# Kernel tuning notes

Hardware: AMD Instinct MI355X
Metric: run time of the kernel (lower is better)

Reference implementation:

```python
import jax, jax.numpy as jnp
import numpy as np

N_NODES = 10000
N_EDGES = 320000
CH = 64          # multiplicity per irrep (64x0e node feats)
R_DIM = 8        # radial embedding dim
L_MAX = 2
N_L = L_MAX + 1
SH_DIM = 9       # 1 + 3 + 5
AVG_NEIGH = 32.0
MLP_HID = 64


def setup_inputs() -> dict:
    key = jax.random.key(0)
    ks = jax.random.split(key, 11)
    return {
        "edge_vectors": jax.random.normal(ks[0], (N_EDGES, 3), jnp.float32),
        "node_feats": jax.random.normal(ks[1], (N_NODES, CH), jnp.float32),
        "radial_embeddings": jax.random.normal(ks[2], (N_EDGES, R_DIM), jnp.float32),
        "senders": jax.random.randint(ks[3], (N_EDGES,), 0, N_NODES),
        "receivers": jax.random.randint(ks[4], (N_EDGES,), 0, N_NODES),
        # learned params (e3nn Linear / MLP weights, unit normal init)
        "W_up": jax.random.normal(ks[5], (CH, CH), jnp.float32),
        "W_mlp1": jax.random.normal(ks[6], (R_DIM, MLP_HID), jnp.float32),
        "W_mlp2": jax.random.normal(ks[7], (MLP_HID, MLP_HID), jnp.float32),
        "W_mlp3": jax.random.normal(ks[8], (MLP_HID, MLP_HID), jnp.float32),
        "W_mlp4": jax.random.normal(ks[9], (MLP_HID, N_L * CH), jnp.float32),
        "W_down": jax.random.normal(ks[10], (N_L, CH, CH), jnp.float32),
    }


def spherical_harmonics(vec):
    """Component-normalized real spherical harmonics (||Y_l||^2 = 2l+1), l=0..2,
    on normalized edge vectors (e3nn normalize=True, normalization='component')."""
    v = vec / jnp.linalg.norm(vec, axis=-1, keepdims=True)
    x, y, z = v[..., 0], v[..., 1], v[..., 2]
    c15 = float(np.sqrt(15.0))
    c5 = float(np.sqrt(5.0))
    sh2 = jnp.stack(
        [c15 * x * y, c15 * y * z, 0.5 * c5 * (3.0 * z * z - 1.0),
         c15 * x * z, 0.5 * c15 * (x * x - y * y)], axis=-1)
    return jnp.concatenate(
        [jnp.ones_like(x)[..., None], float(np.sqrt(3.0)) * v, sh2], axis=-1)  # [E, 9]


def reference(edge_vectors, node_feats, radial_embeddings, senders, receivers,
              W_up, W_mlp1, W_mlp2, W_mlp3, W_mlp4, W_down):
    inv_ch = 1.0 / np.sqrt(CH)
    n_nodes = node_feats.shape[0]

    # linear_up: scalar irreps -> plain channel mixing with e3nn 1/sqrt(fan_in)
    h = (node_feats @ W_up) * inv_ch                               # [N, CH]

    sh = spherical_harmonics(edge_vectors)                         # [E, 9]

    # radial MLP -> one weight per (channel, l) tensor-product path
    m = radial_embeddings
    for W in (W_mlp1, W_mlp2, W_mlp3):
        m = jax.nn.silu((m @ W) / np.sqrt(W.shape[0]))
    mix = (m @ W_mlp4) / np.sqrt(MLP_HID)                          # [E, N_L*CH]
    w = mix.reshape(-1, N_L, CH).transpose(0, 2, 1)                # [E, CH, N_L]
    # broadcast each per-irrep weight over its 2l+1 components
    w = jnp.repeat(w, np.array([1, 3, 5]), axis=-1,
                   total_repeat_length=SH_DIM)                     # [E, CH, 9]

    # tensor product (scalar node feats x Y_l) with radial weights: messages
    msg = h[senders][:, :, None] * sh[:, None, :] * w              # [E, CH, 9]

    # scatter-add to receivers, normalize by avg_num_neighbors
    agg = jax.ops.segment_sum(msg.reshape(msg.shape[0], -1),
                              receivers, num_segments=n_nodes)
    agg = (agg / AVG_NEIGH).reshape(n_nodes, CH, SH_DIM)           # [N, CH, 9]

    # linear_down: independent channel mixing per l (equivariant Linear)
    outs = []
    start = 0
    for l in range(N_L):
        d = 2 * l + 1
        o = jnp.einsum('ncm,cd->ndm', agg[:, :, start:start + d], W_down[l]) * inv_ch
        outs.append(o.reshape(n_nodes, -1))
        start += d
    return jnp.concatenate(outs, axis=-1)                          # [N, 576]
```

## Files before the change

kernel.cpp:

```cpp
#include <hip/hip_runtime.h>
#include <hip/hip_bf16.h>
#include <math.h>

#define N_NODES 10000
#define N_EDGES 320000
#define CH 64
#define MIXW 192
#define EREC 16

#define W1_OFF 0
#define W2_OFF 512
#define W3_OFF 5120
#define W4_OFF 9728
#define W_TOT 23552
#define ACT_STRIDE 72

#define EPB 128

#define PREP_BLKS 92
#define H_BLKS 2500
#define HIST_BLKS 1250

typedef __attribute__((ext_vector_type(8))) short bf16x8;
typedef __attribute__((ext_vector_type(4))) float f32x4;
#define MFMA16(a, b, c) __builtin_amdgcn_mfma_f32_16x16x32_bf16(a, b, c, 0, 0, 0)

__device__ __forceinline__ float bf2f(unsigned short u) {
    union { unsigned int i; float f; } v; v.i = ((unsigned int)u) << 16; return v.f;
}
__device__ __forceinline__ unsigned short f2bf(float f) {
    unsigned int x = __float_as_uint(f);
    unsigned int r = x + 0x7fffu + ((x >> 16) & 1u);
    return (unsigned short)(r >> 16);
}
__device__ __forceinline__ float silu(float t) {
    return t / (1.0f + __expf(-t));
}

__global__ __launch_bounds__(256) void k_pre(const float* __restrict__ W1,
                                             const float* __restrict__ W2,
                                             const float* __restrict__ W3,
                                             const float* __restrict__ W4,
                                             unsigned short* __restrict__ wimg,
                                             const float* __restrict__ nf,
                                             const float* __restrict__ Wup,
                                             float* __restrict__ h,
                                             const int* __restrict__ recv,
                                             int* __restrict__ counts) {
    int bid = blockIdx.x;
    int t = threadIdx.x;
    if (bid < PREP_BLKS) {
        int i = bid * 256 + t;
        if (i >= W_TOT) return;
        float v;
        if (i < W2_OFF) {
            int n = i >> 3, k = i & 7;
            v = W1[k * 64 + n];
        } else if (i < W3_OFF) {
            int j = i - W2_OFF; int n = j / 72, k = j % 72;
            v = (k < 64) ? W2[k * 64 + n] : 0.f;
        } else if (i < W4_OFF) {
            int j = i - W3_OFF; int n = j / 72, k = j % 72;
            v = (k < 64) ? W3[k * 64 + n] : 0.f;
        } else {
            int j = i - W4_OFF; int n = j / 72, k = j % 72;
            v = (k < 64) ? W4[k * MIXW + n] : 0.f;
        }
        wimg[i] = f2bf(v);
    } else if (bid < PREP_BLKS + H_BLKS) {
        int node = __builtin_amdgcn_readfirstlane((bid - PREP_BLKS) * 4 + (t >> 6));
        int lane = t & 63;
        const float* nrow = nf + (size_t)node * CH;
        float acc = 0.f;
#pragma unroll
        for (int k = 0; k < CH; ++k) acc += nrow[k] * Wup[k * CH + lane];
        h[(size_t)node * CH + lane] = acc * 0.125f;
    } else {
        int e = (bid - PREP_BLKS - H_BLKS) * 256 + t;
        atomicAdd(&counts[recv[e]], 1);
    }
}

__global__ __launch_bounds__(1024) void k_scan(const int* __restrict__ counts,
                                               int* __restrict__ offsets,
                                               int* __restrict__ cursor) {
    __shared__ int part[1024];
    int t = threadIdx.x;
    const int CHUNK = 10;
    int base = t * CHUNK;
    int s = 0;
    for (int i = 0; i < CHUNK; ++i) {
        int idx = base + i;
        if (idx < N_NODES) s += counts[idx];
    }
    part[t] = s;
    __syncthreads();
    for (int off = 1; off < 1024; off <<= 1) {
        int v = 0;
        if (t >= off) v = part[t - off];
        __syncthreads();
        part[t] += v;
        __syncthreads();
    }
    int run = part[t] - s;
    for (int i = 0; i < CHUNK; ++i) {
        int idx = base + i;
        if (idx < N_NODES) {
            offsets[idx] = run;
            cursor[idx] = run;
            run += counts[idx];
        }
    }
    if (t == 1023) offsets[N_NODES] = part[1023];
}

__global__ __launch_bounds__(256) void k_scatter(const int* __restrict__ recv,
                                                 int* __restrict__ cursor,
                                                 int* __restrict__ epos) {
    int e = blockIdx.x * 256 + threadIdx.x;
    epos[e] = atomicAdd(&cursor[recv[e]], 1);
}

__global__ __launch_bounds__(256) void k_mlp(const float* __restrict__ ev,
                                             const float* __restrict__ rad,
                                             const unsigned short* __restrict__ wimg,
                                             const int* __restrict__ senders,
                                             const int* __restrict__ epos,
                                             unsigned short* __restrict__ mix,
                                             float* __restrict__ erec) {
    __shared__ unsigned short act[EPB * ACT_STRIDE];
    __shared__ int s_pos[EPB];

    const int t = threadIdx.x;
    const int e0 = blockIdx.x * EPB;
    const int wv = t >> 6;
    const int lane = t & 63;
    const int lrow = lane & 15;
    const int quad = lane >> 4;
    const int wr0 = wv * 32;
    const int em0 = wr0 + lrow;
    const int em1 = em0 + 16;
    const int cr0 = wr0 + quad * 4;
    const int cr1 = cr0 + 16;

    if (lane < 32) s_pos[wr0 + lane] = epos[e0 + wr0 + lane];

    if (t < EPB) {
        int e = e0 + t;
        int p = epos[e];
        float vx = ev[(size_t)e * 3 + 0], vy = ev[(size_t)e * 3 + 1], vz = ev[(size_t)e * 3 + 2];
        float inv = rsqrtf(vx * vx + vy * vy + vz * vz);
        float x = vx * inv, y = vy * inv, z = vz * inv;
        const float s3 = 1.7320508075688772f;
        const float s15 = 3.872983346207417f;
        const float s5 = 2.2360679774997896f;
        float4* rp = (float4*)(erec + (size_t)p * EREC);
        rp[0] = make_float4(1.0f, s3 * x, s3 * y, s3 * z);
        rp[1] = make_float4(s15 * x * y, s15 * y * z, 0.5f * s5 * (3.0f * z * z - 1.0f), s15 * x * z);
        rp[2] = make_float4(0.5f * s15 * (x * x - y * y),
                            __uint_as_float((unsigned)senders[e]), 0.f, 0.f);
        rp[3] = make_float4(0.f, 0.f, 0.f, 0.f);
    }

    bf16x8 ar0 = {0, 0, 0, 0, 0, 0, 0, 0};
    bf16x8 ar1 = {0, 0, 0, 0, 0, 0, 0, 0};
    if (quad == 0) {
        const float4* rp0 = (const float4*)(rad + (size_t)(e0 + em0) * 8);
        const float4* rp1 = (const float4*)(rad + (size_t)(e0 + em1) * 8);
        float4 u = rp0[0], v = rp0[1];
        ar0[0] = (short)f2bf(u.x); ar0[1] = (short)f2bf(u.y);
        ar0[2] = (short)f2bf(u.z); ar0[3] = (short)f2bf(u.w);
        ar0[4] = (short)f2bf(v.x); ar0[5] = (short)f2bf(v.y);
        ar0[6] = (short)f2bf(v.z); ar0[7] = (short)f2bf(v.w);
        u = rp1[0]; v = rp1[1];
        ar1[0] = (short)f2bf(u.x); ar1[1] = (short)f2bf(u.y);
        ar1[2] = (short)f2bf(u.z); ar1[3] = (short)f2bf(u.w);
        ar1[4] = (short)f2bf(v.x); ar1[5] = (short)f2bf(v.y);
        ar1[6] = (short)f2bf(v.z); ar1[7] = (short)f2bf(v.w);
    }

#pragma unroll
    for (int nt = 0; nt < 4; ++nt) {
        bf16x8 bw = {0, 0, 0, 0, 0, 0, 0, 0};
        if (quad == 0) bw = *(const bf16x8*)(wimg + W1_OFF + (nt * 16 + lrow) * 8);
        f32x4 c0 = {0.f, 0.f, 0.f, 0.f};
        f32x4 c1 = {0.f, 0.f, 0.f, 0.f};
        c0 = MFMA16(ar0, bw, c0);
        c1 = MFMA16(ar1, bw, c1);
#pragma unroll
        for (int r = 0; r < 4; ++r) {
            act[(cr0 + r) * ACT_STRIDE + nt * 16 + lrow] =
                (unsigned short)f2bf(silu(c0[r] * 0.3535533905932738f));
            act[(cr1 + r) * ACT_STRIDE + nt * 16 + lrow] =
                (unsigned short)f2bf(silu(c1[r] * 0.3535533905932738f));
        }
    }

#pragma unroll
    for (int L = 0; L < 2; ++L) {
        const unsigned short* wbase = wimg + (L == 0 ? W2_OFF : W3_OFF);
        bf16x8 a00 = *(const bf16x8*)(act + em0 * ACT_STRIDE + quad * 8);
        bf16x8 a01 = *(const bf16x8*)(act + em0 * ACT_STRIDE + 32 + quad * 8);
        bf16x8 a10 = *(const bf16x8*)(act + em1 * ACT_STRIDE + quad * 8);
        bf16x8 a11 = *(const bf16x8*)(act + em1 * ACT_STRIDE + 32 + quad * 8);
        bf16x8 b[4][2];
#pragma unroll
        for (int nt = 0; nt < 4; ++nt)
#pragma unroll
            for (int kh = 0; kh < 2; ++kh)
                b[nt][kh] = *(const bf16x8*)(wbase + (nt * 16 + lrow) * 72 + kh * 32 + quad * 8);
#pragma unroll
        for (int nt = 0; nt < 4; ++nt) {
            f32x4 c0 = {0.f, 0.f, 0.f, 0.f};
            f32x4 c1 = {0.f, 0.f, 0.f, 0.f};
            c0 = MFMA16(a00, b[nt][0], c0);
            c0 = MFMA16(a01, b[nt][1], c0);
            c1 = MFMA16(a10, b[nt][0], c1);
            c1 = MFMA16(a11, b[nt][1], c1);
#pragma unroll
            for (int r = 0; r < 4; ++r) {
                act[(cr0 + r) * ACT_STRIDE + nt * 16 + lrow] =
                    (unsigned short)f2bf(silu(c0[r] * 0.125f));
                act[(cr1 + r) * ACT_STRIDE + nt * 16 + lrow] =
                    (unsigned short)f2bf(silu(c1[r] * 0.125f));
            }
        }
    }

    {
        bf16x8 a00 = *(const bf16x8*)(act + em0 * ACT_STRIDE + quad * 8);
        bf16x8 a01 = *(const bf16x8*)(act + em0 * ACT_STRIDE + 32 + quad * 8);
        bf16x8 a10 = *(const bf16x8*)(act + em1 * ACT_STRIDE + quad * 8);
        bf16x8 a11 = *(const bf16x8*)(act + em1 * ACT_STRIDE + 32 + quad * 8);
#pragma unroll
        for (int T = 0; T < 3; ++T) {
            bf16x8 b[4][2];
#pragma unroll
            for (int ntl = 0; ntl < 4; ++ntl)
#pragma unroll
                for (int kh = 0; kh < 2; ++kh)
                    b[ntl][kh] = *(const bf16x8*)(wimg + W4_OFF +
                        ((T * 4 + ntl) * 16 + lrow) * 72 + kh * 32 + quad * 8);
#pragma unroll
            for (int ntl = 0; ntl < 4; ++ntl) {
                f32x4 c0 = {0.f, 0.f, 0.f, 0.f};
                f32x4 c1 = {0.f, 0.f, 0.f, 0.f};
                c0 = MFMA16(a00, b[ntl][0], c0);
                c0 = MFMA16(a01, b[ntl][1], c0);
                c1 = MFMA16(a10, b[ntl][0], c1);
                c1 = MFMA16(a11, b[ntl][1], c1);
#pragma unroll
                for (int r = 0; r < 4; ++r) {
                    act[(cr0 + r) * ACT_STRIDE + ntl * 16 + lrow] =
                        (unsigned short)f2bf(c0[r] * 0.125f);
                    act[(cr1 + r) * ACT_STRIDE + ntl * 16 + lrow] =
                        (unsigned short)f2bf(c1[r] * 0.125f);
                }
            }
#pragma unroll
            for (int j = 0; j < 4; ++j) {
                int idx = lane + 64 * j;
                int row = idx >> 3, c8 = idx & 7;
                int p = s_pos[wr0 + row];
                uint4 v = *(const uint4*)(act + (wr0 + row) * ACT_STRIDE + c8 * 8);
                *(uint4*)(mix + (size_t)p * MIXW + T * 64 + c8 * 8) = v;
            }
        }
    }
}

__global__ __launch_bounds__(256, 4) void k_aggdown(const int* __restrict__ offsets,
                                                    const float* __restrict__ erec,
                                                    const float* __restrict__ h,
                                                    const unsigned short* __restrict__ mix,
                                                    const float* __restrict__ Wd,
                                                    float* __restrict__ out) {
    __shared__ float sg[4][576];
    int wv = threadIdx.x >> 6;
    int lane = threadIdx.x & 63;
    int node = __builtin_amdgcn_readfirstlane(blockIdx.x * 4 + wv);
    int s0 = __builtin_amdgcn_readfirstlane(offsets[node]);
    int s1 = __builtin_amdgcn_readfirstlane(offsets[node + 1]);
    float acc[9] = {0.f, 0.f, 0.f, 0.f, 0.f, 0.f, 0.f, 0.f, 0.f};
#pragma unroll 4
    for (int i = s0; i < s1; ++i) {
        const float4* rp = (const float4*)(erec + (size_t)i * EREC);
        float4 r0 = rp[0], r1 = rp[1], r2 = rp[2];
        int s = (int)__float_as_uint(r2.y);
        float hv = h[(size_t)s * CH + lane];
        const unsigned short* mrow = mix + (size_t)i * MIXW;
        float w0 = bf2f(mrow[lane]);
        float w1 = bf2f(mrow[64 + lane]);
        float w2 = bf2f(mrow[128 + lane]);
        float h0 = hv * w0, h1 = hv * w1, h2 = hv * w2;
        acc[0] += h0 * r0.x;
        acc[1] += h1 * r0.y;
        acc[2] += h1 * r0.z;
        acc[3] += h1 * r0.w;
        acc[4] += h2 * r1.x;
        acc[5] += h2 * r1.y;
        acc[6] += h2 * r1.z;
        acc[7] += h2 * r1.w;
        acc[8] += h2 * r2.x;
    }
    float* arow = sg[wv];
#pragma unroll
    for (int m = 0; m < 9; ++m) arow[lane * 9 + m] = acc[m] * (1.0f / 32.0f);

    float* orow = out + (size_t)node * 576;
    {
        float a = 0.f;
#pragma unroll
        for (int c = 0; c < 64; ++c) a += arow[c * 9] * Wd[c * 64 + lane];
        orow[lane] = a * 0.125f;
    }
    {
        float m3[3] = {0.f, 0.f, 0.f};
#pragma unroll
        for (int c = 0; c < 64; ++c) {
            float w = Wd[(64 + c) * 64 + lane];
#pragma unroll
            for (int mm = 0; mm < 3; ++mm) m3[mm] += arow[c * 9 + 1 + mm] * w;
        }
#pragma unroll
        for (int mm = 0; mm < 3; ++mm) orow[64 + lane * 3 + mm] = m3[mm] * 0.125f;
    }
    {
        float m5[5] = {0.f, 0.f, 0.f, 0.f, 0.f};
#pragma unroll
        for (int c = 0; c < 64; ++c) {
            float w = Wd[(128 + c) * 64 + lane];
#pragma unroll
            for (int mm = 0; mm < 5; ++mm) m5[mm] += arow[c * 9 + 4 + mm] * w;
        }
#pragma unroll
        for (int mm = 0; mm < 5; ++mm) orow[256 + lane * 5 + mm] = m5[mm] * 0.125f;
    }
}

static inline size_t align256(size_t x) { return (x + 255) & ~(size_t)255; }

extern "C" void kernel_launch(void* const* d_in, const int* in_sizes, int n_in,
                              void* d_out, int out_size, void* d_ws, size_t ws_size,
                              hipStream_t stream) {
    const float* edge_vectors = (const float*)d_in[0];
    const float* node_feats   = (const float*)d_in[1];
    const float* radial       = (const float*)d_in[2];
    const int*   senders      = (const int*)d_in[3];
    const int*   receivers    = (const int*)d_in[4];
    const float* W_up         = (const float*)d_in[5];
    const float* W_mlp1       = (const float*)d_in[6];
    const float* W_mlp2       = (const float*)d_in[7];
    const float* W_mlp3       = (const float*)d_in[8];
    const float* W_mlp4       = (const float*)d_in[9];
    const float* W_down       = (const float*)d_in[10];
    float* out = (float*)d_out;

    char* base = (char*)d_ws;
    size_t off = 0;
    float* h = (float*)(base + off);              off = align256(off + (size_t)N_NODES * CH * 4);
    unsigned short* mix = (unsigned short*)(base + off); off = align256(off + (size_t)N_EDGES * MIXW * 2);
    float* erec = (float*)(base + off);           off = align256(off + (size_t)N_EDGES * EREC * 4);
    unsigned short* wimg = (unsigned short*)(base + off); off = align256(off + (size_t)W_TOT * 2);
    int* epos = (int*)(base + off);               off = align256(off + (size_t)N_EDGES * 4);
    int* counts = (int*)(base + off);             off = align256(off + (size_t)N_NODES * 4);
    int* offsets = (int*)(base + off);            off = align256(off + (size_t)(N_NODES + 1) * 4);
    int* cursor = (int*)(base + off);             off = align256(off + (size_t)N_NODES * 4);

    hipMemsetAsync(counts, 0, (size_t)N_NODES * 4, stream);

    k_pre<<<PREP_BLKS + H_BLKS + HIST_BLKS, 256, 0, stream>>>(
        W_mlp1, W_mlp2, W_mlp3, W_mlp4, wimg, node_feats, W_up, h, receivers, counts);
    k_scan<<<1, 1024, 0, stream>>>(counts, offsets, cursor);
    k_scatter<<<N_EDGES / 256, 256, 0, stream>>>(receivers, cursor, epos);
    k_mlp<<<N_EDGES / EPB, 256, 0, stream>>>(edge_vectors, radial, wimg, senders, epos,
                                             mix, erec);
    k_aggdown<<<N_NODES / 4, 256, 0, stream>>>(offsets, erec, h, mix, W_down, out);
}
```

Before: 251.6 us.

## Fuse scatter into MLP kernel and premultiply sender features into edge weights

Removes the separate scatter kernel: the MLP kernel now does the atomic cursor increment itself to find each edge's sorted position. It gathers sender node features h into shared memory and multiplies them into the radial-MLP output before the bf16 store. The aggregation kernel no longer performs the random h gather or reads a sender index, and the edge record shrinks from 16 to 12 floats. The trade-off is extra shared memory and gathers in the MLP kernel, plus bf16 rounding of the product h*w instead of w alone.

```diff
diff --git a/kernel.cpp b/kernel.cpp
--- a/kernel.cpp
+++ b/kernel.cpp
@@ -6,7 +6,7 @@
 #define N_EDGES 320000
 #define CH 64
 #define MIXW 192
-#define EREC 16
+#define EREC 12
 
 #define W1_OFF 0
 #define W2_OFF 512
@@ -14,6 +14,7 @@
 #define W4_OFF 9728
 #define W_TOT 23552
 #define ACT_STRIDE 72
+#define HROW_STRIDE 66
 
 #define EPB 128
 
@@ -114,22 +115,19 @@
     if (t == 1023) offsets[N_NODES] = part[1023];
 }
 
-__global__ __launch_bounds__(256) void k_scatter(const int* __restrict__ recv,
-                                                 int* __restrict__ cursor,
-                                                 int* __restrict__ epos) {
-    int e = blockIdx.x * 256 + threadIdx.x;
-    epos[e] = atomicAdd(&cursor[recv[e]], 1);
-}
-
 __global__ __launch_bounds__(256) void k_mlp(const float* __restrict__ ev,
                                              const float* __restrict__ rad,
                                              const unsigned short* __restrict__ wimg,
                                              const int* __restrict__ senders,
-                                             const int* __restrict__ epos,
-                                             unsigned short* __restrict__ mix,
+                                             const int* __restrict__ recv,
+                                             int* __restrict__ cursor,
+                                             const float* __restrict__ h,
+                                             unsigned short* __restrict__ hw,
                                              float* __restrict__ erec) {
     __shared__ unsigned short act[EPB * ACT_STRIDE];
+    __shared__ float s_hrow[EPB * HROW_STRIDE];
     __shared__ int s_pos[EPB];
+    __shared__ int s_snd[EPB];
 
     const int t = threadIdx.x;
     const int e0 = blockIdx.x * EPB;
@@ -143,11 +141,11 @@
     const int cr0 = wr0 + quad * 4;
     const int cr1 = cr0 + 16;
 
-    if (lane < 32) s_pos[wr0 + lane] = epos[e0 + wr0 + lane];
-
-    if (t < EPB) {
-        int e = e0 + t;
-        int p = epos[e];
+    if (lane < 32) {
+        int e = e0 + wr0 + lane;
+        int p = atomicAdd(&cursor[recv[e]], 1);
+        s_pos[wr0 + lane] = p;
+        s_snd[wr0 + lane] = senders[e];
         float vx = ev[(size_t)e * 3 + 0], vy = ev[(size_t)e * 3 + 1], vz = ev[(size_t)e * 3 + 2];
         float inv = rsqrtf(vx * vx + vy * vy + vz * vz);
         float x = vx * inv, y = vy * inv, z = vz * inv;
@@ -157,9 +155,13 @@
         float4* rp = (float4*)(erec + (size_t)p * EREC);
         rp[0] = make_float4(1.0f, s3 * x, s3 * y, s3 * z);
         rp[1] = make_float4(s15 * x * y, s15 * y * z, 0.5f * s5 * (3.0f * z * z - 1.0f), s15 * x * z);
-        rp[2] = make_float4(0.5f * s15 * (x * x - y * y),
-                            __uint_as_float((unsigned)senders[e]), 0.f, 0.f);
-        rp[3] = make_float4(0.f, 0.f, 0.f, 0.f);
+        rp[2] = make_float4(0.5f * s15 * (x * x - y * y), 0.f, 0.f, 0.f);
+    }
+
+#pragma unroll
+    for (int j = 0; j < 32; ++j) {
+        int sj = s_snd[wr0 + j];
+        s_hrow[(wr0 + j) * HROW_STRIDE + lane] = h[(size_t)sj * CH + lane];
     }
 
     bf16x8 ar0 = {0, 0, 0, 0, 0, 0, 0, 0};
@@ -232,6 +234,16 @@
         bf16x8 a01 = *(const bf16x8*)(act + em0 * ACT_STRIDE + 32 + quad * 8);
         bf16x8 a10 = *(const bf16x8*)(act + em1 * ACT_STRIDE + quad * 8);
         bf16x8 a11 = *(const bf16x8*)(act + em1 * ACT_STRIDE + 32 + quad * 8);
+
+        float hreg0[4][4], hreg1[4][4];
+#pragma unroll
+        for (int r = 0; r < 4; ++r)
+#pragma unroll
+            for (int ntl = 0; ntl < 4; ++ntl) {
+                hreg0[r][ntl] = s_hrow[(cr0 + r) * HROW_STRIDE + ntl * 16 + lrow];
+                hreg1[r][ntl] = s_hrow[(cr1 + r) * HROW_STRIDE + ntl * 16 + lrow];
+            }
+
 #pragma unroll
         for (int T = 0; T < 3; ++T) {
             bf16x8 b[4][2];
@@ -252,9 +264,9 @@
 #pragma unroll
                 for (int r = 0; r < 4; ++r) {
                     act[(cr0 + r) * ACT_STRIDE + ntl * 16 + lrow] =
-                        (unsigned short)f2bf(c0[r] * 0.125f);
+                        (unsigned short)f2bf(c0[r] * 0.125f * hreg0[r][ntl]);
                     act[(cr1 + r) * ACT_STRIDE + ntl * 16 + lrow] =
-                        (unsigned short)f2bf(c1[r] * 0.125f);
+                        (unsigned short)f2bf(c1[r] * 0.125f * hreg1[r][ntl]);
                 }
             }
 #pragma unroll
@@ -263,7 +275,7 @@
                 int row = idx >> 3, c8 = idx & 7;
                 int p = s_pos[wr0 + row];
                 uint4 v = *(const uint4*)(act + (wr0 + row) * ACT_STRIDE + c8 * 8);
-                *(uint4*)(mix + (size_t)p * MIXW + T * 64 + c8 * 8) = v;
+                *(uint4*)(hw + (size_t)p * MIXW + T * 64 + c8 * 8) = v;
             }
         }
     }
@@ -271,8 +283,7 @@
 
 __global__ __launch_bounds__(256, 4) void k_aggdown(const int* __restrict__ offsets,
                                                     const float* __restrict__ erec,
-                                                    const float* __restrict__ h,
-                                                    const unsigned short* __restrict__ mix,
+                                                    const unsigned short* __restrict__ hw,
                                                     const float* __restrict__ Wd,
                                                     float* __restrict__ out) {
     __shared__ float sg[4][576];
@@ -284,24 +295,20 @@
     float acc[9] = {0.f, 0.f, 0.f, 0.f, 0.f, 0.f, 0.f, 0.f, 0.f};
 #pragma unroll 4
     for (int i = s0; i < s1; ++i) {
-        const float4* rp = (const float4*)(erec + (size_t)i * EREC);
-        float4 r0 = rp[0], r1 = rp[1], r2 = rp[2];
-        int s = (int)__float_as_uint(r2.y);
-        float hv = h[(size_t)s * CH + lane];
-        const unsigned short* mrow = mix + (size_t)i * MIXW;
-        float w0 = bf2f(mrow[lane]);
-        float w1 = bf2f(mrow[64 + lane]);
-        float w2 = bf2f(mrow[128 + lane]);
-        float h0 = hv * w0, h1 = hv * w1, h2 = hv * w2;
-        acc[0] += h0 * r0.x;
-        acc[1] += h1 * r0.y;
-        acc[2] += h1 * r0.z;
-        acc[3] += h1 * r0.w;
-        acc[4] += h2 * r1.x;
-        acc[5] += h2 * r1.y;
-        acc[6] += h2 * r1.z;
-        acc[7] += h2 * r1.w;
-        acc[8] += h2 * r2.x;
+        const float* rp = erec + (size_t)i * EREC;
+        const unsigned short* hrow = hw + (size_t)i * MIXW;
+        float w0 = bf2f(hrow[lane]);
+        float w1 = bf2f(hrow[64 + lane]);
+        float w2 = bf2f(hrow[128 + lane]);
+        acc[0] += w0 * rp[0];
+        acc[1] += w1 * rp[1];
+        acc[2] += w1 * rp[2];
+        acc[3] += w1 * rp[3];
+        acc[4] += w2 * rp[4];
+        acc[5] += w2 * rp[5];
+        acc[6] += w2 * rp[6];
+        acc[7] += w2 * rp[7];
+        acc[8] += w2 * rp[8];
     }
     float* arow = sg[wv];
 #pragma unroll
@@ -359,10 +366,9 @@
     char* base = (char*)d_ws;
     size_t off = 0;
     float* h = (float*)(base + off);              off = align256(off + (size_t)N_NODES * CH * 4);
-    unsigned short* mix = (unsigned short*)(base + off); off = align256(off + (size_t)N_EDGES * MIXW * 2);
+    unsigned short* hw = (unsigned short*)(base + off); off = align256(off + (size_t)N_EDGES * MIXW * 2);
     float* erec = (float*)(base + off);           off = align256(off + (size_t)N_EDGES * EREC * 4);
     unsigned short* wimg = (unsigned short*)(base + off); off = align256(off + (size_t)W_TOT * 2);
-    int* epos = (int*)(base + off);               off = align256(off + (size_t)N_EDGES * 4);
     int* counts = (int*)(base + off);             off = align256(off + (size_t)N_NODES * 4);
     int* offsets = (int*)(base + off);            off = align256(off + (size_t)(N_NODES + 1) * 4);
     int* cursor = (int*)(base + off);             off = align256(off + (size_t)N_NODES * 4);
@@ -372,8 +378,7 @@
     k_pre<<<PREP_BLKS + H_BLKS + HIST_BLKS, 256, 0, stream>>>(
         W_mlp1, W_mlp2, W_mlp3, W_mlp4, wimg, node_feats, W_up, h, receivers, counts);
     k_scan<<<1, 1024, 0, stream>>>(counts, offsets, cursor);
-    k_scatter<<<N_EDGES / 256, 256, 0, stream>>>(receivers, cursor, epos);
-    k_mlp<<<N_EDGES / EPB, 256, 0, stream>>>(edge_vectors, radial, wimg, senders, epos,
-                                             mix, erec);
-    k_aggdown<<<N_NODES / 4, 256, 0, stream>>>(offsets, erec, h, mix, W_down, out);
-}
+    k_mlp<<<N_EDGES / EPB, 256, 0, stream>>>(edge_vectors, radial, wimg, senders,
+                                             receivers, cursor, h, hw, erec);
+    k_aggdown<<<N_NODES / 4, 256, 0, stream>>>(offsets, erec, hw, W_down, out);
+}
```

Measured after the change: 230.4 us. -8.4%, faster.
